# Kernel optimization log

Hardware: AMD Instinct MI355X
Metric: run time of the kernel (lower is better)

The kernel has to match this reference:

```python
import jax, jax.numpy as jnp
import numpy as np

HEADS = 8
EMBED = 512
D_K = EMBED // HEADS
B, S = 2, 4096


def setup_inputs() -> dict:
    key = jax.random.key(0)
    ks = jax.random.split(key, 12)
    sc = 1.0 / np.sqrt(EMBED)
    inp = {
        "query": jax.random.normal(ks[0], (B, S, EMBED), jnp.float32),
        "key": jax.random.normal(ks[1], (B, S, EMBED), jnp.float32),
        "value": jax.random.normal(ks[2], (B, S, EMBED), jnp.float32),
        # causal (decoder) mask, broadcast over batch and heads
        "mask": jnp.tril(jnp.ones((S, S), jnp.int32))[None, None, :, :],
        "Wq": jax.random.normal(ks[3], (EMBED, EMBED), jnp.float32) * sc,
        "bq": jnp.zeros((EMBED,), jnp.float32),
        "Wk": jax.random.normal(ks[4], (EMBED, EMBED), jnp.float32) * sc,
        "bk": jnp.zeros((EMBED,), jnp.float32),
        "Wv": jax.random.normal(ks[5], (EMBED, EMBED), jnp.float32) * sc,
        "bv": jnp.zeros((EMBED,), jnp.float32),
        "Wo": jax.random.normal(ks[6], (EMBED, EMBED), jnp.float32) * sc,
        "bo": jnp.zeros((EMBED,), jnp.float32),
    }
    return inp


def reference(query, key, value, mask, Wq, bq, Wk, bk, Wv, bv, Wo, bo):
    b, s, e = query.shape
    # linear projections (torch Linear: x @ W.T + b)
    q = query @ Wq.T + bq
    k = key @ Wk.T + bk
    v = value @ Wv.T + bv
    # [b, h, s, d_k]
    q = q.reshape(b, s, HEADS, D_K).transpose(0, 2, 1, 3)
    k = k.reshape(b, s, HEADS, D_K).transpose(0, 2, 1, 3)
    v = v.reshape(b, s, HEADS, D_K).transpose(0, 2, 1, 3)
    scores = jnp.einsum("bhqd,bhkd->bhqk", q, k) / jnp.sqrt(jnp.float32(D_K))
    scores = jnp.where(mask == 0, jnp.float32(-1e20), scores)
    attn = jax.nn.softmax(scores, axis=-1)  # dropout is identity in eval
    ctx = jnp.einsum("bhqk,bhkd->bhqd", attn, v)
    ctx = ctx.transpose(0, 2, 1, 3).reshape(b, s, e)
    return ctx @ Wo.T + bo
```

## Files before the change

kernel.cpp:

```cpp
#include <hip/hip_runtime.h>
#include <hip/hip_bf16.h>

#define HEADS 8
#define DK    64
#define SEQ   4096
#define EMB   512
#define BATCH 2

using f32x4  = __attribute__((ext_vector_type(4))) float;
using f32x16 = __attribute__((ext_vector_type(16))) float;
using bf16x8 = __attribute__((ext_vector_type(8))) short;
using uint2v = __attribute__((ext_vector_type(2))) uint;

union frg { uint u[4]; bf16x8 v; };

__device__ __forceinline__ ushort f2bf(float f) {
    union { float f; uint32_t u; } x{f};
    uint32_t r = (x.u + 0x7fff + ((x.u >> 16) & 1)) >> 16;
    return (ushort)r;
}

__device__ __forceinline__ uint pk2(float a, float b) {
    __hip_bfloat162 h = __float22bfloat162_rn(make_float2(a, b));
    union { __hip_bfloat162 h; uint u; } c; c.h = h; return c.u;
}

__device__ __forceinline__ uint2v pswap(uint a, uint b) {
    return __builtin_amdgcn_permlane32_swap(a, b, false, false);
}

__device__ __forceinline__ void gld16(const ushort* g, short* l) {
    __builtin_amdgcn_global_load_lds(
        (const __attribute__((address_space(1))) void*)g,
        (__attribute__((address_space(3))) void*)l, 16, 0, 0);
}

__global__ __launch_bounds__(256) void gemm_qkv(
    const float* __restrict__ Aq, const float* __restrict__ Ak, const float* __restrict__ Av,
    const float* __restrict__ Wq, const float* __restrict__ Wk, const float* __restrict__ Wv,
    const float* __restrict__ bq, const float* __restrict__ bk, const float* __restrict__ bv,
    ushort* __restrict__ Qb, ushort* __restrict__ Kb, ushort* __restrict__ Vb)
{
    const int z = blockIdx.z;
    const float* A    = z == 0 ? Aq : z == 1 ? Ak : Av;
    const float* W    = z == 0 ? Wq : z == 1 ? Wk : Wv;
    const float* bias = z == 0 ? bq : z == 1 ? bk : bv;
    ushort* out       = z == 0 ? Qb : z == 1 ? Kb : Vb;
    const float osc   = z == 0 ? 0.125f * 1.44269504089f : 1.0f;

    const int Kd = EMB;
    __shared__ short As[128][40];
    __shared__ short Bs[128][40];

    const int tid = threadIdx.x;
    const int wave = tid >> 6, lane = tid & 63;
    const int wm = wave >> 1, wn = wave & 1;
    const int lr = lane & 15, lg = lane >> 4;
    const int m0 = blockIdx.x * 128, n0 = blockIdx.y * 128;

    f32x4 acc[4][4] = {};

    for (int k0 = 0; k0 < Kd; k0 += 32) {
        #pragma unroll
        for (int i = 0; i < 4; ++i) {
            int idx4 = tid + i * 256;
            int r = idx4 >> 3, c = (idx4 & 7) * 4;
            float4 va = *(const float4*)(A + (size_t)(m0 + r) * Kd + k0 + c);
            ushort4 ha;
            ha.x = f2bf(va.x); ha.y = f2bf(va.y); ha.z = f2bf(va.z); ha.w = f2bf(va.w);
            *(ushort4*)(&As[r][c]) = ha;
            float4 vb2 = *(const float4*)(W + (size_t)(n0 + r) * Kd + k0 + c);
            ushort4 hb;
            hb.x = f2bf(vb2.x); hb.y = f2bf(vb2.y); hb.z = f2bf(vb2.z); hb.w = f2bf(vb2.w);
            *(ushort4*)(&Bs[r][c]) = hb;
        }
        __syncthreads();

        bf16x8 a[4], bfr[4];
        #pragma unroll
        for (int i = 0; i < 4; ++i)
            a[i] = *(const bf16x8*)(&As[wm * 64 + i * 16 + lr][lg * 8]);
        #pragma unroll
        for (int i = 0; i < 4; ++i)
            bfr[i] = *(const bf16x8*)(&Bs[wn * 64 + i * 16 + lr][lg * 8]);

        #pragma unroll
        for (int mi = 0; mi < 4; ++mi)
            #pragma unroll
            for (int ni = 0; ni < 4; ++ni)
                acc[mi][ni] = __builtin_amdgcn_mfma_f32_16x16x32_bf16(
                    a[mi], bfr[ni], acc[mi][ni], 0, 0, 0);
        __syncthreads();
    }

    #pragma unroll
    for (int ni = 0; ni < 4; ++ni) {
        const int n = n0 + wn * 64 + ni * 16 + lr;
        const float bv2 = bias[n];
        #pragma unroll
        for (int mi = 0; mi < 4; ++mi) {
            #pragma unroll
            for (int j = 0; j < 4; ++j) {
                const int mm = m0 + wm * 64 + mi * 16 + lg * 4 + j;
                float v = (acc[mi][ni][j] + bv2) * osc;
                const int b = mm >> 12, s = mm & (SEQ - 1);
                const int h = n >> 6,  d = n & (DK - 1);
                size_t off;
                if (z == 2) off = ((size_t)(b * HEADS + h) * DK  + d) * SEQ + s;
                else        off = ((size_t)(b * HEADS + h) * SEQ + s) * DK + d;
                out[off] = f2bf(v);
            }
        }
    }
}

__global__ __launch_bounds__(256) void gemm_out(
    const ushort* __restrict__ Ab, const float* __restrict__ W,
    const float* __restrict__ bias, float* __restrict__ out)
{
    const int N = EMB, Kd = EMB;
    __shared__ short As[128][40];
    __shared__ short Bs[128][40];

    const int tid = threadIdx.x;
    const int wave = tid >> 6, lane = tid & 63;
    const int wm = wave >> 1, wn = wave & 1;
    const int lr = lane & 15, lg = lane >> 4;
    const int m0 = blockIdx.x * 128, n0 = blockIdx.y * 128;

    f32x4 acc[4][4] = {};

    for (int k0 = 0; k0 < Kd; k0 += 32) {
        #pragma unroll
        for (int i = 0; i < 2; ++i) {
            int idx8 = tid + i * 256;
            int r = idx8 >> 2, c = (idx8 & 3) * 8;
            bf16x8 v = *(const bf16x8*)(Ab + (size_t)(m0 + r) * Kd + k0 + c);
            *(bf16x8*)(&As[r][c]) = v;
        }
        #pragma unroll
        for (int i = 0; i < 4; ++i) {
            int idx4 = tid + i * 256;
            int r = idx4 >> 3, c = (idx4 & 7) * 4;
            float4 v = *(const float4*)(W + (size_t)(n0 + r) * Kd + k0 + c);
            ushort4 hb;
            hb.x = f2bf(v.x); hb.y = f2bf(v.y); hb.z = f2bf(v.z); hb.w = f2bf(v.w);
            *(ushort4*)(&Bs[r][c]) = hb;
        }
        __syncthreads();

        bf16x8 a[4], bfr[4];
        #pragma unroll
        for (int i = 0; i < 4; ++i)
            a[i] = *(const bf16x8*)(&As[wm * 64 + i * 16 + lr][lg * 8]);
        #pragma unroll
        for (int i = 0; i < 4; ++i)
            bfr[i] = *(const bf16x8*)(&Bs[wn * 64 + i * 16 + lr][lg * 8]);

        #pragma unroll
        for (int mi = 0; mi < 4; ++mi)
            #pragma unroll
            for (int ni = 0; ni < 4; ++ni)
                acc[mi][ni] = __builtin_amdgcn_mfma_f32_16x16x32_bf16(
                    a[mi], bfr[ni], acc[mi][ni], 0, 0, 0);
        __syncthreads();
    }

    #pragma unroll
    for (int ni = 0; ni < 4; ++ni) {
        const int n = n0 + wn * 64 + ni * 16 + lr;
        const float bv = bias[n];
        #pragma unroll
        for (int mi = 0; mi < 4; ++mi)
            #pragma unroll
            for (int j = 0; j < 4; ++j) {
                const int mm = m0 + wm * 64 + mi * 16 + lg * 4 + j;
                out[(size_t)mm * N + n] = acc[mi][ni][j] + bv;
            }
    }
}

__global__ __launch_bounds__(256) void attn9(
    const ushort* __restrict__ Q, const ushort* __restrict__ K,
    const ushort* __restrict__ Vt, ushort* __restrict__ ctx)
{
    __shared__ short kv[2][2][64][64];

    const int tid  = threadIdx.x;
    const int wave = tid >> 6, lane = tid & 63;
    const int ql = lane & 31, hi = lane >> 5;

    const int bid  = blockIdx.x;
    const int xcd  = bid & 7;
    const int s    = bid >> 3;
    const int bh   = (xcd << 1) | (s & 1);
    const int qblk = 31 - (s >> 1);
    const int q0b  = qblk * 128;
    const int q0w  = q0b + wave * 32;
    const int b = bh >> 3, h = bh & 7;
    const int qg = q0w + ql;

    const ushort* Qp = Q  + ((size_t)bh * SEQ + q0w) * DK;
    const ushort* Kp = K  + (size_t)bh * SEQ * DK;
    const ushort* Vp = Vt + (size_t)bh * DK * SEQ;

    bf16x8 qf[4];
    #pragma unroll
    for (int ks = 0; ks < 4; ++ks)
        qf[ks] = *(const bf16x8*)(Qp + ql * DK + ks * 16 + hi * 8);

    bf16x8 ones;
    #pragma unroll
    for (int i = 0; i < 8; ++i) ones[i] = (short)0x3F80;

    f32x16 oa0 = {}, oa1 = {};
    f32x16 oaL = {};

    const int ntmax = q0b / 64 + 2;
    const int ntw   = (q0w + 31) / 64 + 1;

    auto stage = [&](int buf, int t) {
        const int r0 = wave * 16;
        const int rr = lane >> 3;
        const int c  = lane & 7;
        #pragma unroll
        for (int i = 0; i < 2; ++i) {
            int row = r0 + i * 8 + rr;
            gld16(Kp + (size_t)(t * 64 + row) * DK + ((c ^ (row & 7)) << 3),
                  &kv[buf][0][r0 + i * 8][0]);
        }
        #pragma unroll
        for (int i = 0; i < 2; ++i) {
            int row = r0 + i * 8 + rr;
            gld16(Vp + (size_t)row * SEQ + t * 64 + ((c ^ (row & 7)) << 3),
                  &kv[buf][1][r0 + i * 8][0]);
        }
    };

    const int swz = (ql & 7) << 4;

    auto compute = [&](int buf, int kv0, bool masked) {
        const char* kb = (const char*)&kv[buf][0][0][0];
        const char* vb = (const char*)&kv[buf][1][0][0];

        f32x16 s0, s1;
        #pragma unroll
        for (int r = 0; r < 16; ++r) { s0[r] = -20.0f; s1[r] = -20.0f; }
        #pragma unroll
        for (int ks = 0; ks < 4; ++ks) {
            bf16x8 kf = *(const bf16x8*)(kb + ql * 128 + (((ks * 2 + hi) << 4) ^ swz));
            s0 = __builtin_amdgcn_mfma_f32_32x32x16_bf16(kf, qf[ks], s0, 0, 0, 0);
        }
        #pragma unroll
        for (int ks = 0; ks < 4; ++ks) {
            bf16x8 kf = *(const bf16x8*)(kb + (32 + ql) * 128 + (((ks * 2 + hi) << 4) ^ swz));
            s1 = __builtin_amdgcn_mfma_f32_32x32x16_bf16(kf, qf[ks], s1, 0, 0, 0);
        }

        if (masked) {
            #pragma unroll
            for (int r = 0; r < 16; ++r) {
                int kvg = kv0 + (r & 3) + 8 * (r >> 2) + 4 * hi;
                if (kvg      > qg) s0[r] = -3e38f;
                if (kvg + 32 > qg) s1[r] = -3e38f;
            }
        }

        #pragma unroll
        for (int r = 0; r < 16; ++r) {
            s0[r] = exp2f(s0[r]);
            s1[r] = exp2f(s1[r]);
        }

        frg f0, f1, f2, f3;
        {
            uint w01 = pk2(s0[0], s0[1]),   w23 = pk2(s0[2], s0[3]);
            uint w45 = pk2(s0[4], s0[5]),   w67 = pk2(s0[6], s0[7]);
            uint w89 = pk2(s0[8], s0[9]),   wab = pk2(s0[10], s0[11]);
            uint wcd = pk2(s0[12], s0[13]), wef = pk2(s0[14], s0[15]);
            uint2v p0 = pswap(w01, w45), p1 = pswap(w23, w67);
            uint2v p2 = pswap(w89, wcd), p3 = pswap(wab, wef);
            f0.u[0] = p0[0]; f0.u[1] = p1[0]; f0.u[2] = p0[1]; f0.u[3] = p1[1];
            f1.u[0] = p2[0]; f1.u[1] = p3[0]; f1.u[2] = p2[1]; f1.u[3] = p3[1];
        }
        {
            uint w01 = pk2(s1[0], s1[1]),   w23 = pk2(s1[2], s1[3]);
            uint w45 = pk2(s1[4], s1[5]),   w67 = pk2(s1[6], s1[7]);
            uint w89 = pk2(s1[8], s1[9]),   wab = pk2(s1[10], s1[11]);
            uint wcd = pk2(s1[12], s1[13]), wef = pk2(s1[14], s1[15]);
            uint2v p0 = pswap(w01, w45), p1 = pswap(w23, w67);
            uint2v p2 = pswap(w89, wcd), p3 = pswap(wab, wef);
            f2.u[0] = p0[0]; f2.u[1] = p1[0]; f2.u[2] = p0[1]; f2.u[3] = p1[1];
            f3.u[0] = p2[0]; f3.u[1] = p3[0]; f3.u[2] = p2[1]; f3.u[3] = p3[1];
        }

        #pragma unroll
        for (int sl = 0; sl < 4; ++sl) {
            const frg* fp = sl == 0 ? &f0 : sl == 1 ? &f1 : sl == 2 ? &f2 : &f3;
            bf16x8 v0 = *(const bf16x8*)(vb + ql * 128        + (((sl * 2 + hi) << 4) ^ swz));
            bf16x8 v1 = *(const bf16x8*)(vb + (32 + ql) * 128 + (((sl * 2 + hi) << 4) ^ swz));
            oa0 = __builtin_amdgcn_mfma_f32_32x32x16_bf16(v0, fp->v, oa0, 0, 0, 0);
            oa1 = __builtin_amdgcn_mfma_f32_32x32x16_bf16(v1, fp->v, oa1, 0, 0, 0);
            oaL = __builtin_amdgcn_mfma_f32_32x32x16_bf16(ones, fp->v, oaL, 0, 0, 0);
        }
    };

    stage(0, 0);
    int cur = 0;
    for (int t = 0; t < ntmax; ++t) {
        if (t + 1 < ntmax) {
            stage(cur ^ 1, t + 1);
            asm volatile("s_waitcnt vmcnt(4)" ::: "memory");
        } else {
            asm volatile("s_waitcnt vmcnt(0)" ::: "memory");
        }
        __builtin_amdgcn_sched_barrier(0);
        __builtin_amdgcn_s_barrier();
        if (t < ntw)
            compute(cur, t * 64, t == ntw - 1);
        __builtin_amdgcn_s_barrier();
        cur ^= 1;
    }

    const float rinv = 1.0f / oaL[0];
    ushort* crow = ctx + ((size_t)b * SEQ + qg) * EMB + h * DK;
    #pragma unroll
    for (int g = 0; g < 4; ++g) {
        ushort4 p;
        p.x = f2bf(oa0[g * 4 + 0] * rinv); p.y = f2bf(oa0[g * 4 + 1] * rinv);
        p.z = f2bf(oa0[g * 4 + 2] * rinv); p.w = f2bf(oa0[g * 4 + 3] * rinv);
        *(ushort4*)(crow + g * 8 + hi * 4) = p;
    }
    #pragma unroll
    for (int g = 0; g < 4; ++g) {
        ushort4 p;
        p.x = f2bf(oa1[g * 4 + 0] * rinv); p.y = f2bf(oa1[g * 4 + 1] * rinv);
        p.z = f2bf(oa1[g * 4 + 2] * rinv); p.w = f2bf(oa1[g * 4 + 3] * rinv);
        *(ushort4*)(crow + 32 + g * 8 + hi * 4) = p;
    }
}

extern "C" void kernel_launch(void* const* d_in, const int* in_sizes, int n_in,
                              void* d_out, int out_size, void* d_ws, size_t ws_size,
                              hipStream_t stream) {
    const float* query = (const float*)d_in[0];
    const float* key   = (const float*)d_in[1];
    const float* value = (const float*)d_in[2];
    const float* Wq = (const float*)d_in[4];
    const float* bq = (const float*)d_in[5];
    const float* Wk = (const float*)d_in[6];
    const float* bk = (const float*)d_in[7];
    const float* Wv = (const float*)d_in[8];
    const float* bv = (const float*)d_in[9];
    const float* Wo = (const float*)d_in[10];
    const float* bo = (const float*)d_in[11];

    const size_t MK = (size_t)BATCH * SEQ * EMB;
    ushort* Qb = (ushort*)d_ws;
    ushort* Kb = Qb + MK;
    ushort* Vb = Kb + MK;
    ushort* Cb = Vb + MK;

    gemm_qkv<<<dim3(64, 4, 3), 256, 0, stream>>>(query, key, value,
                                                 Wq, Wk, Wv, bq, bk, bv,
                                                 Qb, Kb, Vb);
    attn9<<<dim3(512), 256, 0, stream>>>(Qb, Kb, Vb, Cb);
    gemm_out<<<dim3(64, 4), 256, 0, stream>>>(Cb, Wo, bo, (float*)d_out);
}
```

Baseline: 159.2 us.

## Split causal attention along KV into segments with atomic partial accumulation

Each attention block now covers one of up to four 16-tile KV segments of its query block, which raises the grid from 512 to 1280 blocks and evens out the causal load imbalance. Unnormalized partial outputs and row sums go to a zeroed fp32 workspace through atomicAdd, and normalization plus bf16 conversion move into the output GEMM's A-tile load. This adds a zeroing kernel, many fp32 atomics, and twice the traffic for the intermediate context. The design is only correct if every segment uses the same fixed softmax max; the code appears to rely on exp2 without a running max, which would make it consistent.

```diff
diff --git a/kernel.cpp b/kernel.cpp
--- a/kernel.cpp
+++ b/kernel.cpp
@@ -33,6 +33,12 @@
     __builtin_amdgcn_global_load_lds(
         (const __attribute__((address_space(1))) void*)g,
         (__attribute__((address_space(3))) void*)l, 16, 0, 0);
+}
+
+__global__ void zero_ws(float4* __restrict__ p, int n4) {
+    int stride = gridDim.x * blockDim.x;
+    for (int i = blockIdx.x * blockDim.x + threadIdx.x; i < n4; i += stride)
+        p[i] = make_float4(0.f, 0.f, 0.f, 0.f);
 }
 
 __global__ __launch_bounds__(256) void gemm_qkv(
@@ -115,8 +121,9 @@
 }
 
 __global__ __launch_bounds__(256) void gemm_out(
-    const ushort* __restrict__ Ab, const float* __restrict__ W,
-    const float* __restrict__ bias, float* __restrict__ out)
+    const float* __restrict__ Op, const float* __restrict__ Lp,
+    const float* __restrict__ W, const float* __restrict__ bias,
+    float* __restrict__ out)
 {
     const int N = EMB, Kd = EMB;
     __shared__ short As[128][40];
@@ -132,19 +139,23 @@
 
     for (int k0 = 0; k0 < Kd; k0 += 32) {
         #pragma unroll
-        for (int i = 0; i < 2; ++i) {
-            int idx8 = tid + i * 256;
-            int r = idx8 >> 2, c = (idx8 & 3) * 8;
-            bf16x8 v = *(const bf16x8*)(Ab + (size_t)(m0 + r) * Kd + k0 + c);
-            *(bf16x8*)(&As[r][c]) = v;
-        }
-        #pragma unroll
         for (int i = 0; i < 4; ++i) {
             int idx4 = tid + i * 256;
             int r = idx4 >> 3, c = (idx4 & 7) * 4;
-            float4 v = *(const float4*)(W + (size_t)(n0 + r) * Kd + k0 + c);
+            int mm = m0 + r;
+            int bb = mm >> 12, ss = mm & (SEQ - 1);
+            int k = k0 + c;
+            int bh = bb * 8 + (k >> 6), d = k & 63;
+            float4 v = *(const float4*)(Op + ((size_t)bh * SEQ + ss) * 64 + d);
+            float rl = 1.0f / Lp[(size_t)bh * SEQ + ss];
+            ushort4 ha;
+            ha.x = f2bf(v.x * rl); ha.y = f2bf(v.y * rl);
+            ha.z = f2bf(v.z * rl); ha.w = f2bf(v.w * rl);
+            *(ushort4*)(&As[r][c]) = ha;
+
+            float4 vb2 = *(const float4*)(W + (size_t)(n0 + r) * Kd + k0 + c);
             ushort4 hb;
-            hb.x = f2bf(v.x); hb.y = f2bf(v.y); hb.z = f2bf(v.z); hb.w = f2bf(v.w);
+            hb.x = f2bf(vb2.x); hb.y = f2bf(vb2.y); hb.z = f2bf(vb2.z); hb.w = f2bf(vb2.w);
             *(ushort4*)(&Bs[r][c]) = hb;
         }
         __syncthreads();
@@ -180,9 +191,10 @@
     }
 }
 
-__global__ __launch_bounds__(256) void attn9(
+__global__ __launch_bounds__(256) void attn10(
     const ushort* __restrict__ Q, const ushort* __restrict__ K,
-    const ushort* __restrict__ Vt, ushort* __restrict__ ctx)
+    const ushort* __restrict__ Vt,
+    float* __restrict__ Op, float* __restrict__ Lp)
 {
     __shared__ short kv[2][2][64][64];
 
@@ -190,15 +202,26 @@
     const int wave = tid >> 6, lane = tid & 63;
     const int ql = lane & 31, hi = lane >> 5;
 
-    const int bid  = blockIdx.x;
-    const int xcd  = bid & 7;
-    const int s    = bid >> 3;
-    const int bh   = (xcd << 1) | (s & 1);
-    const int qblk = 31 - (s >> 1);
-    const int q0b  = qblk * 128;
-    const int q0w  = q0b + wave * 32;
-    const int b = bh >> 3, h = bh & 7;
-    const int qg = q0w + ql;
+    const int bid = blockIdx.x;
+    const int xcd = bid & 7;
+    const int idx = bid >> 3;
+    const int p   = idx & 1;
+    const int j   = idx >> 1;
+    int qblk, seg;
+    if (j < 32)      { qblk = 31 - (j >> 2);      seg = j & 3; }
+    else if (j < 56) { int jj = j - 32; int d3 = jj / 3; qblk = 23 - d3; seg = jj - d3 * 3; }
+    else if (j < 72) { int jj = j - 56; qblk = 15 - (jj >> 1); seg = jj & 1; }
+    else             { qblk = 7 - (j - 72);       seg = 0; }
+    const int bh = xcd * 2 + p;
+
+    const int q0b = qblk * 128;
+    const int q0w = q0b + wave * 32;
+    const int qg  = q0w + ql;
+
+    const int ntchunk = 2 * qblk + 2;
+    const int t_begin = seg * 16;
+    const int t_end   = min(t_begin + 16, ntchunk);
+    const int ntw     = (q0w + 31) / 64 + 1;
 
     const ushort* Qp = Q  + ((size_t)bh * SEQ + q0w) * DK;
     const ushort* Kp = K  + (size_t)bh * SEQ * DK;
@@ -215,9 +238,6 @@
 
     f32x16 oa0 = {}, oa1 = {};
     f32x16 oaL = {};
-
-    const int ntmax = q0b / 64 + 2;
-    const int ntw   = (q0w + 31) / 64 + 1;
 
     auto stage = [&](int buf, int t) {
         const int r0 = wave * 16;
@@ -305,10 +325,10 @@
         }
     };
 
-    stage(0, 0);
+    stage(0, t_begin);
     int cur = 0;
-    for (int t = 0; t < ntmax; ++t) {
-        if (t + 1 < ntmax) {
+    for (int t = t_begin; t < t_end; ++t) {
+        if (t + 1 < t_end) {
             stage(cur ^ 1, t + 1);
             asm volatile("s_waitcnt vmcnt(4)" ::: "memory");
         } else {
@@ -322,22 +342,16 @@
         cur ^= 1;
     }
 
-    const float rinv = 1.0f / oaL[0];
-    ushort* crow = ctx + ((size_t)b * SEQ + qg) * EMB + h * DK;
-    #pragma unroll
-    for (int g = 0; g < 4; ++g) {
-        ushort4 p;
-        p.x = f2bf(oa0[g * 4 + 0] * rinv); p.y = f2bf(oa0[g * 4 + 1] * rinv);
-        p.z = f2bf(oa0[g * 4 + 2] * rinv); p.w = f2bf(oa0[g * 4 + 3] * rinv);
-        *(ushort4*)(crow + g * 8 + hi * 4) = p;
-    }
-    #pragma unroll
-    for (int g = 0; g < 4; ++g) {
-        ushort4 p;
-        p.x = f2bf(oa1[g * 4 + 0] * rinv); p.y = f2bf(oa1[g * 4 + 1] * rinv);
-        p.z = f2bf(oa1[g * 4 + 2] * rinv); p.w = f2bf(oa1[g * 4 + 3] * rinv);
-        *(ushort4*)(crow + 32 + g * 8 + hi * 4) = p;
-    }
+    float* orow = Op + ((size_t)bh * SEQ + qg) * 64;
+    #pragma unroll
+    for (int g = 0; g < 4; ++g)
+        #pragma unroll
+        for (int jj = 0; jj < 4; ++jj) {
+            atomicAdd(orow + g * 8 + hi * 4 + jj,      oa0[g * 4 + jj]);
+            atomicAdd(orow + 32 + g * 8 + hi * 4 + jj, oa1[g * 4 + jj]);
+        }
+    if (hi == 0)
+        atomicAdd(Lp + (size_t)bh * SEQ + qg, oaL[0]);
 }
 
 extern "C" void kernel_launch(void* const* d_in, const int* in_sizes, int n_in,
@@ -359,11 +373,14 @@
     ushort* Qb = (ushort*)d_ws;
     ushort* Kb = Qb + MK;
     ushort* Vb = Kb + MK;
-    ushort* Cb = Vb + MK;
-
+    float*  Op = (float*)(Vb + MK);
+    float*  Lp = Op + (size_t)BATCH * HEADS * SEQ * DK;
+
+    const int n4 = (int)((BATCH * HEADS * SEQ * DK + BATCH * HEADS * SEQ) / 4);
+    zero_ws<<<dim3(1024), 256, 0, stream>>>((float4*)Op, n4);
     gemm_qkv<<<dim3(64, 4, 3), 256, 0, stream>>>(query, key, value,
                                                  Wq, Wk, Wv, bq, bk, bv,
                                                  Qb, Kb, Vb);
-    attn9<<<dim3(512), 256, 0, stream>>>(Qb, Kb, Vb, Cb);
-    gemm_out<<<dim3(64, 4), 256, 0, stream>>>(Cb, Wo, bo, (float*)d_out);
-}
+    attn10<<<dim3(1280), 256, 0, stream>>>(Qb, Kb, Vb, Op, Lp);
+    gemm_out<<<dim3(64, 4), 256, 0, stream>>>(Op, Lp, Wo, bo, (float*)d_out);
+}
```

Result: slower. 353.5 us (+122.1%).
